# Kernel tuning notes

Measured on AMD Instinct MI355X. Metric: run time of the kernel, lower is better.

The kernel has to match this reference:

```python
import jax, jax.numpy as jnp
import numpy as np

B, S, H = 2, 2048, 4096
NH, NKV, HD = 32, 8, 128
GROUPS = NH // NKV
ROPE_THETA = 10000.0


def _rotate_half(x):
    x1, x2 = jnp.split(x, 2, axis=-1)
    return jnp.concatenate([-x2, x1], axis=-1)


def setup_inputs() -> dict:
    key = jax.random.key(0)
    k1, k2 = jax.random.split(key, 2)
    hidden_states = jax.random.normal(k1, (B, S, H), dtype=jnp.float32)
    position_ids = jnp.tile(jnp.arange(S, dtype=jnp.int64)[None, :], (B, 1))
    # rotary tables, llama-style: freqs duplicated into full head_dim
    inv_freq = (1.0 / (ROPE_THETA ** (np.arange(0, HD, 2, dtype=np.float32) / HD))).astype(np.float32)
    ang = position_ids[..., None].astype(jnp.float32) * jnp.asarray(inv_freq)  # (B,S,HD/2)
    emb = jnp.concatenate([ang, ang], axis=-1)  # (B,S,HD)
    cos = jnp.cos(emb)
    sin = jnp.sin(emb)
    # fused QKV weight, stored as (in, out) so x @ w matches Linear(x)
    w_qkv = jax.random.normal(k2, (H, (NH + 2 * NKV) * HD), dtype=jnp.float32) * 0.02
    return {"hidden_states": hidden_states, "cos": cos, "sin": sin,
            "w_qkv": w_qkv, "position_ids": position_ids}


def reference(hidden_states, cos, sin, w_qkv, position_ids):
    bsz, q_len, _ = hidden_states.shape
    q_slice = NH * HD
    k_slice = q_slice + NKV * HD
    # fused QKV gemm
    qkv = hidden_states @ w_qkv  # (B,S,(NH+2*NKV)*HD)
    query = qkv[:, :, :q_slice].reshape(bsz, q_len, NH, HD)
    key = qkv[:, :, q_slice:k_slice].reshape(bsz, q_len, NKV, HD)
    value = qkv[:, :, k_slice:].reshape(bsz, q_len, NKV, HD)
    # RoPE (broadcast cos/sin over head axis)
    c = cos[:, :, None, :]
    s = sin[:, :, None, :]
    query = query * c + _rotate_half(query) * s
    key = key * c + _rotate_half(key) * s
    # (B, heads, S, HD)
    q = query.transpose(0, 2, 1, 3)
    k = jnp.repeat(key.transpose(0, 2, 1, 3), GROUPS, axis=1)
    v = jnp.repeat(value.transpose(0, 2, 1, 3), GROUPS, axis=1)
    scale = 1.0 / jnp.sqrt(jnp.asarray(HD, dtype=q.dtype))
    scores = jnp.einsum("bhqd,bhkd->bhqk", q, k) * scale
    causal = jnp.tril(jnp.ones((q_len, q_len), dtype=bool))
    scores = jnp.where(causal[None, None], scores, jnp.asarray(-1e30, scores.dtype))
    probs = jax.nn.softmax(scores, axis=-1)
    attn = jnp.einsum("bhqk,bhkd->bhqd", probs, v)  # (B,NH,S,HD)
    out = attn.transpose(0, 2, 1, 3).reshape(bsz, q_len, NH * HD)
    return out
```

## Files before the change

kernel.cpp:

```cpp
#include <hip/hip_runtime.h>
#include <hip/hip_bf16.h>

#define BATCH 2
#define S_LEN 2048
#define HID   4096
#define N_QKV 6144
#define NHEADS 32
#define NKVH   8
#define HDIM   128
#define MROWS  4096
#define QBLK  128
#define KVBLK 64

typedef __attribute__((ext_vector_type(4))) float f32x4;
typedef __attribute__((ext_vector_type(8))) short bf16x8;
typedef __attribute__((ext_vector_type(4))) short bf16x4;

__device__ __forceinline__ unsigned short f2bf(float f) {
    unsigned int u = __float_as_uint(f);
    u += 0x7FFFu + ((u >> 16) & 1u);
    return (unsigned short)(u >> 16);
}
__device__ __forceinline__ float bf2f(unsigned short v) {
    return __uint_as_float(((unsigned int)v) << 16);
}

__global__ void cvt_bf16_kernel(const float* __restrict__ in, unsigned short* __restrict__ out) {
    size_t i = ((size_t)blockIdx.x * 256 + threadIdx.x) * 4;
    f32x4 v = *(const f32x4*)(in + i);
    bf16x4 o;
    o.x = (short)f2bf(v.x); o.y = (short)f2bf(v.y);
    o.z = (short)f2bf(v.z); o.w = (short)f2bf(v.w);
    *(bf16x4*)(out + i) = o;
}

__global__ void transpose_w_kernel(const float* __restrict__ w, unsigned short* __restrict__ wt) {
    __shared__ unsigned short tile[64][72];
    const int tn = blockIdx.x * 64;
    const int tk = blockIdx.y * 64;
    const int t  = threadIdx.x;
    const int c4 = (t & 15) * 4;
    const int rr = t >> 4;
#pragma unroll
    for (int i = 0; i < 4; i++) {
        int k = rr + i * 16;
        f32x4 v = *(const f32x4*)(w + (size_t)(tk + k) * N_QKV + tn + c4);
        tile[k][c4 + 0] = f2bf(v.x);
        tile[k][c4 + 1] = f2bf(v.y);
        tile[k][c4 + 2] = f2bf(v.z);
        tile[k][c4 + 3] = f2bf(v.w);
    }
    __syncthreads();
#pragma unroll
    for (int i = 0; i < 4; i++) {
        int n = rr + i * 16;
        bf16x4 o;
        o.x = (short)tile[c4 + 0][n];
        o.y = (short)tile[c4 + 1][n];
        o.z = (short)tile[c4 + 2][n];
        o.w = (short)tile[c4 + 3][n];
        *(bf16x4*)(wt + (size_t)(tn + n) * HID + tk + c4) = o;
    }
}

__device__ __forceinline__ void gload_lds16(const unsigned short* g, unsigned short* l) {
    __builtin_amdgcn_global_load_lds(
        (const __attribute__((address_space(1))) unsigned int*)g,
        (__attribute__((address_space(3))) unsigned int*)l, 16, 0, 0);
}

__global__ __launch_bounds__(256) void gemm_qkv_kernel(const unsigned short* __restrict__ A,
                                                       const unsigned short* __restrict__ Bt,
                                                       unsigned short* __restrict__ C) {
    __shared__ unsigned short Al[128 * 32];
    __shared__ unsigned short Bl[128 * 32];
    const int bm = (blockIdx.x & 31) * 128;
    const int bn = (blockIdx.x >> 5) * 128;
    const int t = threadIdx.x;
    const int w = t >> 6, l = t & 63;
    const int wm = (w >> 1) * 64, wn = (w & 1) * 64;
    f32x4 acc[4][4] = {};

    const int srow = w * 32 + (l >> 2);
    const int skk  = (l & 3) * 8;
    const unsigned short* ag = A  + (size_t)(bm + srow) * HID + skk;
    const unsigned short* bg = Bt + (size_t)(bn + srow) * HID + skk;

    for (int k0 = 0; k0 < HID; k0 += 32) {
#pragma unroll
        for (int c = 0; c < 2; c++) {
            gload_lds16(ag + (size_t)c * 16 * HID + k0, Al + (w * 32 + c * 16) * 32);
            gload_lds16(bg + (size_t)c * 16 * HID + k0, Bl + (w * 32 + c * 16) * 32);
        }
        __syncthreads();
        bf16x8 af[4], bfr[4];
#pragma unroll
        for (int i = 0; i < 4; i++) {
            af[i]  = *(const bf16x8*)(Al + (wm + i * 16 + (l & 15)) * 32 + (l >> 4) * 8);
            bfr[i] = *(const bf16x8*)(Bl + (wn + i * 16 + (l & 15)) * 32 + (l >> 4) * 8);
        }
#pragma unroll
        for (int i = 0; i < 4; i++)
#pragma unroll
            for (int j = 0; j < 4; j++)
                acc[i][j] = __builtin_amdgcn_mfma_f32_16x16x32_bf16(af[i], bfr[j], acc[i][j], 0, 0, 0);
        __syncthreads();
    }

#pragma unroll
    for (int i = 0; i < 4; i++)
#pragma unroll
        for (int j = 0; j < 4; j++)
#pragma unroll
            for (int r = 0; r < 4; r++) {
                int row = bm + wm + i * 16 + (l >> 4) * 4 + r;
                int col = bn + wn + j * 16 + (l & 15);
                C[(size_t)row * N_QKV + col] = f2bf(acc[i][j][r]);
            }
}

__global__ void rope_kernel(unsigned short* __restrict__ qkv,
                            const float* __restrict__ cs, const float* __restrict__ sn) {
    size_t id = (size_t)blockIdx.x * 256 + threadIdx.x;
    int d = (int)(id & 63);
    size_t tmp = id >> 6;
    int hd = (int)(tmp % 40);
    size_t r = tmp / 40;
    float c = cs[r * HDIM + d];
    float s = sn[r * HDIM + d];
    unsigned short* p = qkv + r * N_QKV + (size_t)hd * HDIM + d;
    float x1 = bf2f(p[0]), x2 = bf2f(p[64]);
    float o1 = x1 * c - x2 * s;
    float o2 = x2 * c + x1 * s;
    if (hd < NHEADS) { o1 *= 0.088388347648318447f; o2 *= 0.088388347648318447f; }
    p[0]  = f2bf(o1);
    p[64] = f2bf(o2);
}

__global__ void transpose_v_kernel(const unsigned short* __restrict__ qkv,
                                   unsigned short* __restrict__ vtg) {
    __shared__ unsigned short tile[64][72];
    const int bz = blockIdx.z;
    const int d0 = blockIdx.y * 64;
    const int s0 = blockIdx.x * 64;
    const int b  = bz >> 3, kvh = bz & 7;
    const int t = threadIdx.x;
#pragma unroll
    for (int i = 0; i < 2; i++) {
        int s  = i * 32 + (t >> 3);
        int dl = (t & 7) * 8;
        bf16x8 v = *(const bf16x8*)(qkv + (size_t)(b * S_LEN + s0 + s) * N_QKV
                                    + HID + NKVH * HDIM + (size_t)kvh * HDIM + d0 + dl);
        *(bf16x8*)(&tile[s][dl]) = v;
    }
    __syncthreads();
#pragma unroll
    for (int i = 0; i < 2; i++) {
        int d  = i * 32 + (t >> 3);
        int sl = (t & 7) * 8;
        bf16x8 o;
#pragma unroll
        for (int j = 0; j < 8; j++) o[j] = (short)tile[sl + j][d];
        *(bf16x8*)(vtg + ((size_t)bz * HDIM + d0 + d) * S_LEN + s0 + sl) = o;
    }
}

__global__ __launch_bounds__(256, 2) void attn_kernel(const unsigned short* __restrict__ qkv,
                                                      const unsigned short* __restrict__ vtg,
                                                      float* __restrict__ out) {
    __shared__ unsigned short Kl[2][KVBLK * HDIM];
    __shared__ unsigned short Vl[HDIM * KVBLK];
    __shared__ unsigned short Pl[4][16 * 72];

    const int bid = blockIdx.x;
    const int qbi = bid & 15;
    const int h   = (bid >> 4) & 31;
    const int b   = bid >> 9;
    const int kvh = h >> 2;
    const int qb  = qbi * QBLK;
    const int t = threadIdx.x, w = t >> 6, l = t & 63;
    const int lo = l & 15, hi = l >> 4;
    const int sw = lo & 7;
    const size_t rowb = (size_t)b * S_LEN;

    const int krow = t >> 4;
    const unsigned short* kg = qkv + (rowb + krow) * N_QKV + HID + (size_t)kvh * HDIM
                               + (((t & 15) ^ (krow & 7)) << 3);
    const int vrow = t >> 3;
    const unsigned short* vg = vtg + ((size_t)(b * NKVH + kvh) * HDIM + vrow) * S_LEN
                               + (((t & 7) ^ (vrow & 7)) << 3);
    unsigned short* kl0 = &Kl[0][t * 8];
    unsigned short* kl1 = &Kl[1][t * 8];
    unsigned short* vl  = &Vl[t * 8];

    bf16x8 qf[2][4];
#pragma unroll
    for (int g = 0; g < 2; g++) {
        const unsigned short* qp = qkv + (rowb + qb + w * 32 + g * 16 + lo) * N_QKV
                                   + (size_t)h * HDIM + hi * 8;
#pragma unroll
        for (int kc = 0; kc < 4; kc++) qf[g][kc] = *(const bf16x8*)(qp + kc * 32);
    }

    f32x4 of[2][8] = {};
    float m_r[2][4], l_r[2][4];
#pragma unroll
    for (int g = 0; g < 2; g++)
#pragma unroll
        for (int r = 0; r < 4; r++) { m_r[g][r] = -1e30f; l_r[g][r] = 0.f; }

    const int nt = (qb + QBLK) / KVBLK;
    const int wrowmax = qb + w * 32 + 31;

#pragma unroll
    for (int i = 0; i < 4; i++)
        gload_lds16(kg + (size_t)i * 16 * N_QKV, kl0 + i * 2048);

    for (int kt = 0; kt < nt; kt++) {
        const int kv0 = kt * KVBLK;
        __syncthreads();
#pragma unroll
        for (int i = 0; i < 4; i++)
            gload_lds16(vg + kv0 + (size_t)i * 32 * S_LEN, vl + i * 2048);
        if (kt + 1 < nt) {
            const unsigned short* kp = kg + (size_t)(kv0 + KVBLK) * N_QKV;
            unsigned short* kd = ((kt + 1) & 1) ? kl1 : kl0;
#pragma unroll
            for (int i = 0; i < 4; i++)
                gload_lds16(kp + (size_t)i * 16 * N_QKV, kd + i * 2048);
        }

        bf16x8 pf[2][2];
        const bool wact = (kv0 <= wrowmax);
        if (wact) {
            const unsigned short* Kb = (kt & 1) ? &Kl[1][0] : &Kl[0][0];
            f32x4 sf[2][4] = {};
#pragma unroll
            for (int kvb = 0; kvb < 4; kvb++)
#pragma unroll
                for (int kc = 0; kc < 4; kc++) {
                    bf16x8 kf = *(const bf16x8*)(Kb + (kvb * 16 + lo) * HDIM
                                                 + (((kc * 4 + hi) ^ sw) << 3));
#pragma unroll
                    for (int g = 0; g < 2; g++)
                        sf[g][kvb] = __builtin_amdgcn_mfma_f32_16x16x32_bf16(
                            qf[g][kc], kf, sf[g][kvb], 0, 0, 0);
                }
#pragma unroll
            for (int g = 0; g < 2; g++) {
                const int rb = qb + w * 32 + g * 16;
                if (kv0 + KVBLK - 1 > rb) {
#pragma unroll
                    for (int kvb = 0; kvb < 4; kvb++) {
                        const int kv = kv0 + kvb * 16 + lo;
#pragma unroll
                        for (int r = 0; r < 4; r++)
                            if (kv > rb + hi * 4 + r) sf[g][kvb][r] = -1e30f;
                    }
                }
                float pm[4];
#pragma unroll
                for (int r = 0; r < 4; r++)
                    pm[r] = fmaxf(fmaxf(sf[g][0][r], sf[g][1][r]),
                                  fmaxf(sf[g][2][r], sf[g][3][r]));
#pragma unroll
                for (int off = 8; off >= 1; off >>= 1)
#pragma unroll
                    for (int r = 0; r < 4; r++)
                        pm[r] = fmaxf(pm[r], __shfl_xor(pm[r], off, 64));
                float dm = fmaxf(fmaxf(pm[0] - m_r[g][0], pm[1] - m_r[g][1]),
                                 fmaxf(pm[2] - m_r[g][2], pm[3] - m_r[g][3]));
                if (__any(dm > 8.0f)) {
#pragma unroll
                    for (int r = 0; r < 4; r++) {
                        const float mn = fmaxf(m_r[g][r], pm[r]);
                        const float sc = __expf(m_r[g][r] - mn);
                        m_r[g][r] = mn;
                        l_r[g][r] *= sc;
#pragma unroll
                        for (int d16 = 0; d16 < 8; d16++) of[g][d16][r] *= sc;
                    }
                }
                float rs[4] = {0.f, 0.f, 0.f, 0.f};
#pragma unroll
                for (int kvb = 0; kvb < 4; kvb++)
#pragma unroll
                    for (int r = 0; r < 4; r++) {
                        const float p = __expf(sf[g][kvb][r] - m_r[g][r]);
                        sf[g][kvb][r] = p;
                        rs[r] += p;
                    }
#pragma unroll
                for (int off = 8; off >= 1; off >>= 1)
#pragma unroll
                    for (int r = 0; r < 4; r++) rs[r] += __shfl_xor(rs[r], off, 64);
#pragma unroll
                for (int r = 0; r < 4; r++) l_r[g][r] += rs[r];
                unsigned short* Pw = &Pl[w][0];
#pragma unroll
                for (int kvb = 0; kvb < 4; kvb++)
#pragma unroll
                    for (int r = 0; r < 4; r++)
                        Pw[(hi * 4 + r) * 72 + kvb * 16 + lo] = f2bf(sf[g][kvb][r]);
#pragma unroll
                for (int kh = 0; kh < 2; kh++)
                    pf[g][kh] = *(const bf16x8*)(Pw + lo * 72 + kh * 32 + hi * 8);
            }
        }
        __syncthreads();
        if (wact) {
#pragma unroll
            for (int kh = 0; kh < 2; kh++)
#pragma unroll
                for (int d16 = 0; d16 < 8; d16++) {
                    bf16x8 vf = *(const bf16x8*)(&Vl[0]
                                                 + ((d16 * 16 + lo) << 6)
                                                 + (((kh * 4 + hi) ^ sw) << 3));
#pragma unroll
                    for (int g = 0; g < 2; g++)
                        of[g][d16] = __builtin_amdgcn_mfma_f32_16x16x32_bf16(
                            pf[g][kh], vf, of[g][d16], 0, 0, 0);
                }
        }
    }

#pragma unroll
    for (int g = 0; g < 2; g++) {
        float inv[4];
#pragma unroll
        for (int r = 0; r < 4; r++) inv[r] = 1.0f / l_r[g][r];
        const size_t rb = rowb + qb + w * 32 + g * 16 + hi * 4;
#pragma unroll
        for (int d16 = 0; d16 < 8; d16++)
#pragma unroll
            for (int r = 0; r < 4; r++)
                out[(rb + r) * HID + (size_t)h * HDIM + d16 * 16 + lo] = of[g][d16][r] * inv[r];
    }
}

extern "C" void kernel_launch(void* const* d_in, const int* in_sizes, int n_in,
                              void* d_out, int out_size, void* d_ws, size_t ws_size,
                              hipStream_t stream) {
    const float* hidden = (const float*)d_in[0];
    const float* cosb   = (const float*)d_in[1];
    const float* sinb   = (const float*)d_in[2];
    const float* w_qkv  = (const float*)d_in[3];

    unsigned short* hbf = (unsigned short*)d_ws;
    unsigned short* wt  = hbf + (size_t)MROWS * HID;
    unsigned short* qkv = wt + (size_t)N_QKV * HID;
    unsigned short* vtg = (unsigned short*)d_ws;
    float* out = (float*)d_out;

    cvt_bf16_kernel<<<(MROWS * (size_t)HID) / 1024, 256, 0, stream>>>(hidden, hbf);
    transpose_w_kernel<<<dim3(N_QKV / 64, HID / 64), 256, 0, stream>>>(w_qkv, wt);
    gemm_qkv_kernel<<<(MROWS / 128) * (N_QKV / 128), 256, 0, stream>>>(hbf, wt, qkv);
    rope_kernel<<<((size_t)MROWS * 40 * 64) / 256, 256, 0, stream>>>(qkv, cosb, sinb);
    transpose_v_kernel<<<dim3(S_LEN / 64, HDIM / 64, BATCH * NKVH), 256, 0, stream>>>(qkv, vtg);
    attn_kernel<<<BATCH * NHEADS * (S_LEN / QBLK), 256, 0, stream>>>(qkv, vtg, out);
}
```

Measured before the change: 711.3 us.

## Rewrite QKV GEMM as 256x256 pipelined tile and pair causal attention query blocks

The QKV GEMM moves from 128x128 tiles with 256 threads to 256x256 tiles with 512 threads. It uses double-buffered, XOR-swizzled LDS staging with explicit vmcnt waits, barrier-interleaved phases, setprio around MFMA bursts, and a grid swizzle for L2 locality. This targets the GEMM's memory-latency and LDS-reload overhead, at the cost of 128KB of LDS and more registers per block. Separately, each attention block now processes query block i and its mirror 15-i, which balances causal work across blocks and halves the grid.

```diff
diff --git a/kernel.cpp b/kernel.cpp
--- a/kernel.cpp
+++ b/kernel.cpp
@@ -11,6 +11,7 @@
 #define MROWS  4096
 #define QBLK  128
 #define KVBLK 64
+#define NT_K  64
 
 typedef __attribute__((ext_vector_type(4))) float f32x4;
 typedef __attribute__((ext_vector_type(8))) short bf16x8;
@@ -69,52 +70,103 @@
         (__attribute__((address_space(3))) unsigned int*)l, 16, 0, 0);
 }
 
-__global__ __launch_bounds__(256) void gemm_qkv_kernel(const unsigned short* __restrict__ A,
-                                                       const unsigned short* __restrict__ Bt,
-                                                       unsigned short* __restrict__ C) {
-    __shared__ unsigned short Al[128 * 32];
-    __shared__ unsigned short Bl[128 * 32];
-    const int bm = (blockIdx.x & 31) * 128;
-    const int bn = (blockIdx.x >> 5) * 128;
+__global__ __launch_bounds__(512, 2) void gemm_qkv_kernel(const unsigned short* __restrict__ A,
+                                                          const unsigned short* __restrict__ Bt,
+                                                          unsigned short* __restrict__ C) {
+    __shared__ alignas(16) unsigned short AL[32768];
+    __shared__ alignas(16) unsigned short BL[32768];
     const int t = threadIdx.x;
     const int w = t >> 6, l = t & 63;
-    const int wm = (w >> 1) * 64, wn = (w & 1) * 64;
-    f32x4 acc[4][4] = {};
-
-    const int srow = w * 32 + (l >> 2);
-    const int skk  = (l & 3) * 8;
-    const unsigned short* ag = A  + (size_t)(bm + srow) * HID + skk;
-    const unsigned short* bg = Bt + (size_t)(bn + srow) * HID + skk;
-
-    for (int k0 = 0; k0 < HID; k0 += 32) {
-#pragma unroll
-        for (int c = 0; c < 2; c++) {
-            gload_lds16(ag + (size_t)c * 16 * HID + k0, Al + (w * 32 + c * 16) * 32);
-            gload_lds16(bg + (size_t)c * 16 * HID + k0, Bl + (w * 32 + c * 16) * 32);
-        }
-        __syncthreads();
-        bf16x8 af[4], bfr[4];
-#pragma unroll
-        for (int i = 0; i < 4; i++) {
-            af[i]  = *(const bf16x8*)(Al + (wm + i * 16 + (l & 15)) * 32 + (l >> 4) * 8);
-            bfr[i] = *(const bf16x8*)(Bl + (wn + i * 16 + (l & 15)) * 32 + (l >> 4) * 8);
-        }
-#pragma unroll
-        for (int i = 0; i < 4; i++)
-#pragma unroll
-            for (int j = 0; j < 4; j++)
-                acc[i][j] = __builtin_amdgcn_mfma_f32_16x16x32_bf16(af[i], bfr[j], acc[i][j], 0, 0, 0);
-        __syncthreads();
-    }
-
-#pragma unroll
-    for (int i = 0; i < 4; i++)
+    const int lo = l & 15, hi = l >> 4;
+    const int wr = w >> 2, wc = w & 3;
+    const int bid = blockIdx.x;
+    const int swz = (bid & 7) * 48 + (bid >> 3);
+    const int bm = (swz / 24) * 256;
+    const int bn = (swz % 24) * 256;
+
+    const int rS = t >> 2;
+    const int cS = (t & 3) ^ ((rS >> 1) & 3);
+    const unsigned short* As = A  + (size_t)(bm + rS) * HID + cS * 8;
+    const unsigned short* Bs = Bt + (size_t)(bn + rS) * HID + cS * 8;
+    unsigned short* ALd = AL + t * 8;
+    unsigned short* BLd = BL + t * 8;
+
+#define STAGE_A(DST, KPOS) do { \
+        gload_lds16(As + (KPOS), ALd + (DST)); \
+        gload_lds16(As + (size_t)128 * HID + (KPOS), ALd + (DST) + 4096); } while (0)
+#define STAGE_B(DST, KPOS) do { \
+        gload_lds16(Bs + (KPOS), BLd + (DST)); \
+        gload_lds16(Bs + (size_t)128 * HID + (KPOS), BLd + (DST) + 4096); } while (0)
+
+    STAGE_A(0, 0);            STAGE_B(0, 0);
+    STAGE_A(8192, 32);        STAGE_B(8192, 32);
+    STAGE_A(16384, 64);       STAGE_B(16384, 64);
+    asm volatile("s_waitcnt vmcnt(8)" ::: "memory");
+    __builtin_amdgcn_s_barrier();
+
+    f32x4 acc[8][4] = {};
+    const int csw8 = (hi ^ ((l & 6) >> 1)) * 8;
+
+#define GPHASE(KHB, MH, READB, STAGECODE, WAITCODE) do {                         \
+        bf16x8 af0, af1, af2, af3;                                               \
+        { const unsigned short* ap = Ab + (KHB) + (wr * 128 + (MH) * 64 + lo) * 32 + csw8; \
+          af0 = *(const bf16x8*)(ap);                                            \
+          af1 = *(const bf16x8*)(ap + 16 * 32);                                  \
+          af2 = *(const bf16x8*)(ap + 32 * 32);                                  \
+          af3 = *(const bf16x8*)(ap + 48 * 32); }                                \
+        if (READB) {                                                             \
+          const unsigned short* bp = Bb + (KHB) + (wc * 64 + lo) * 32 + csw8;    \
+          bfr[0] = *(const bf16x8*)(bp);                                         \
+          bfr[1] = *(const bf16x8*)(bp + 16 * 32);                               \
+          bfr[2] = *(const bf16x8*)(bp + 32 * 32);                               \
+          bfr[3] = *(const bf16x8*)(bp + 48 * 32); }                             \
+        STAGECODE;                                                               \
+        __builtin_amdgcn_s_barrier();                                            \
+        __builtin_amdgcn_s_setprio(1);                                           \
+        _Pragma("unroll")                                                        \
+        for (int jj = 0; jj < 4; jj++) {                                         \
+            acc[(MH)*4+0][jj] = __builtin_amdgcn_mfma_f32_16x16x32_bf16(af0, bfr[jj], acc[(MH)*4+0][jj], 0, 0, 0); \
+            acc[(MH)*4+1][jj] = __builtin_amdgcn_mfma_f32_16x16x32_bf16(af1, bfr[jj], acc[(MH)*4+1][jj], 0, 0, 0); \
+            acc[(MH)*4+2][jj] = __builtin_amdgcn_mfma_f32_16x16x32_bf16(af2, bfr[jj], acc[(MH)*4+2][jj], 0, 0, 0); \
+            acc[(MH)*4+3][jj] = __builtin_amdgcn_mfma_f32_16x16x32_bf16(af3, bfr[jj], acc[(MH)*4+3][jj], 0, 0, 0); \
+        }                                                                        \
+        __builtin_amdgcn_s_setprio(0);                                           \
+        WAITCODE;                                                                \
+        __builtin_amdgcn_s_barrier();                                            \
+    } while (0)
+
+    for (int u = 0; u < NT_K; u++) {
+        const int buf = (u & 1) * 16384;
+        const unsigned short* Ab = AL + buf;
+        const unsigned short* Bb = BL + buf;
+        bf16x8 bfr[4];
+        GPHASE(0, 0, 1,
+               { if (u + 1 < NT_K) STAGE_A(((u + 1) & 1) * 16384 + 8192, (u + 1) * 64 + 32); },
+               {});
+        GPHASE(0, 1, 0,
+               { if (u + 1 < NT_K) STAGE_B(((u + 1) & 1) * 16384 + 8192, (u + 1) * 64 + 32); },
+               { if (u < NT_K - 1) asm volatile("s_waitcnt vmcnt(8)" ::: "memory");
+                 else              asm volatile("s_waitcnt vmcnt(0)" ::: "memory"); });
+        GPHASE(8192, 0, 1,
+               { if (u + 2 < NT_K) STAGE_A(buf, (u + 2) * 64); },
+               {});
+        GPHASE(8192, 1, 0,
+               { if (u + 2 < NT_K) STAGE_B(buf, (u + 2) * 64); },
+               { if (u < NT_K - 2)      asm volatile("s_waitcnt vmcnt(8)" ::: "memory");
+                 else if (u == NT_K - 2) asm volatile("s_waitcnt vmcnt(4)" ::: "memory"); });
+    }
+#undef GPHASE
+#undef STAGE_A
+#undef STAGE_B
+
+#pragma unroll
+    for (int i = 0; i < 8; i++)
 #pragma unroll
         for (int j = 0; j < 4; j++)
 #pragma unroll
             for (int r = 0; r < 4; r++) {
-                int row = bm + wm + i * 16 + (l >> 4) * 4 + r;
-                int col = bn + wn + j * 16 + (l & 15);
+                const int row = bm + wr * 128 + i * 16 + hi * 4 + r;
+                const int col = bn + wc * 64 + j * 16 + lo;
                 C[(size_t)row * N_QKV + col] = f2bf(acc[i][j][r]);
             }
 }
@@ -173,11 +225,10 @@
     __shared__ unsigned short Pl[4][16 * 72];
 
     const int bid = blockIdx.x;
-    const int qbi = bid & 15;
-    const int h   = (bid >> 4) & 31;
-    const int b   = bid >> 9;
+    const int qbi0 = bid & 7;
+    const int h   = (bid >> 3) & 31;
+    const int b   = bid >> 8;
     const int kvh = h >> 2;
-    const int qb  = qbi * QBLK;
     const int t = threadIdx.x, w = t >> 6, l = t & 63;
     const int lo = l & 15, hi = l >> 4;
     const int sw = lo & 7;
@@ -193,148 +244,152 @@
     unsigned short* kl1 = &Kl[1][t * 8];
     unsigned short* vl  = &Vl[t * 8];
 
-    bf16x8 qf[2][4];
-#pragma unroll
-    for (int g = 0; g < 2; g++) {
-        const unsigned short* qp = qkv + (rowb + qb + w * 32 + g * 16 + lo) * N_QKV
-                                   + (size_t)h * HDIM + hi * 8;
-#pragma unroll
-        for (int kc = 0; kc < 4; kc++) qf[g][kc] = *(const bf16x8*)(qp + kc * 32);
-    }
-
-    f32x4 of[2][8] = {};
-    float m_r[2][4], l_r[2][4];
-#pragma unroll
-    for (int g = 0; g < 2; g++)
-#pragma unroll
-        for (int r = 0; r < 4; r++) { m_r[g][r] = -1e30f; l_r[g][r] = 0.f; }
-
-    const int nt = (qb + QBLK) / KVBLK;
-    const int wrowmax = qb + w * 32 + 31;
-
-#pragma unroll
-    for (int i = 0; i < 4; i++)
-        gload_lds16(kg + (size_t)i * 16 * N_QKV, kl0 + i * 2048);
-
-    for (int kt = 0; kt < nt; kt++) {
-        const int kv0 = kt * KVBLK;
-        __syncthreads();
+    for (int hv = 0; hv < 2; hv++) {
+        const int qb = (hv ? (15 - qbi0) : qbi0) * QBLK;
+
+        bf16x8 qf[2][4];
+#pragma unroll
+        for (int g = 0; g < 2; g++) {
+            const unsigned short* qp = qkv + (rowb + qb + w * 32 + g * 16 + lo) * N_QKV
+                                       + (size_t)h * HDIM + hi * 8;
+#pragma unroll
+            for (int kc = 0; kc < 4; kc++) qf[g][kc] = *(const bf16x8*)(qp + kc * 32);
+        }
+
+        f32x4 of[2][8] = {};
+        float m_r[2][4], l_r[2][4];
+#pragma unroll
+        for (int g = 0; g < 2; g++)
+#pragma unroll
+            for (int r = 0; r < 4; r++) { m_r[g][r] = -1e30f; l_r[g][r] = 0.f; }
+
+        const int nt = (qb + QBLK) / KVBLK;
+        const int wrowmax = qb + w * 32 + 31;
+
 #pragma unroll
         for (int i = 0; i < 4; i++)
-            gload_lds16(vg + kv0 + (size_t)i * 32 * S_LEN, vl + i * 2048);
-        if (kt + 1 < nt) {
-            const unsigned short* kp = kg + (size_t)(kv0 + KVBLK) * N_QKV;
-            unsigned short* kd = ((kt + 1) & 1) ? kl1 : kl0;
+            gload_lds16(kg + (size_t)i * 16 * N_QKV, kl0 + i * 2048);
+
+        for (int kt = 0; kt < nt; kt++) {
+            const int kv0 = kt * KVBLK;
+            __syncthreads();
 #pragma unroll
             for (int i = 0; i < 4; i++)
-                gload_lds16(kp + (size_t)i * 16 * N_QKV, kd + i * 2048);
-        }
-
-        bf16x8 pf[2][2];
-        const bool wact = (kv0 <= wrowmax);
-        if (wact) {
-            const unsigned short* Kb = (kt & 1) ? &Kl[1][0] : &Kl[0][0];
-            f32x4 sf[2][4] = {};
-#pragma unroll
-            for (int kvb = 0; kvb < 4; kvb++)
-#pragma unroll
-                for (int kc = 0; kc < 4; kc++) {
-                    bf16x8 kf = *(const bf16x8*)(Kb + (kvb * 16 + lo) * HDIM
-                                                 + (((kc * 4 + hi) ^ sw) << 3));
-#pragma unroll
-                    for (int g = 0; g < 2; g++)
-                        sf[g][kvb] = __builtin_amdgcn_mfma_f32_16x16x32_bf16(
-                            qf[g][kc], kf, sf[g][kvb], 0, 0, 0);
+                gload_lds16(vg + kv0 + (size_t)i * 32 * S_LEN, vl + i * 2048);
+            if (kt + 1 < nt) {
+                const unsigned short* kp = kg + (size_t)(kv0 + KVBLK) * N_QKV;
+                unsigned short* kd = ((kt + 1) & 1) ? kl1 : kl0;
+#pragma unroll
+                for (int i = 0; i < 4; i++)
+                    gload_lds16(kp + (size_t)i * 16 * N_QKV, kd + i * 2048);
+            }
+
+            bf16x8 pf[2][2];
+            const bool wact = (kv0 <= wrowmax);
+            if (wact) {
+                const unsigned short* Kb = (kt & 1) ? &Kl[1][0] : &Kl[0][0];
+                f32x4 sf[2][4] = {};
+#pragma unroll
+                for (int kvb = 0; kvb < 4; kvb++)
+#pragma unroll
+                    for (int kc = 0; kc < 4; kc++) {
+                        bf16x8 kf = *(const bf16x8*)(Kb + (kvb * 16 + lo) * HDIM
+                                                     + (((kc * 4 + hi) ^ sw) << 3));
+#pragma unroll
+                        for (int g = 0; g < 2; g++)
+                            sf[g][kvb] = __builtin_amdgcn_mfma_f32_16x16x32_bf16(
+                                qf[g][kc], kf, sf[g][kvb], 0, 0, 0);
+                    }
+#pragma unroll
+                for (int g = 0; g < 2; g++) {
+                    const int rb = qb + w * 32 + g * 16;
+                    if (kv0 + KVBLK - 1 > rb) {
+#pragma unroll
+                        for (int kvb = 0; kvb < 4; kvb++) {
+                            const int kv = kv0 + kvb * 16 + lo;
+#pragma unroll
+                            for (int r = 0; r < 4; r++)
+                                if (kv > rb + hi * 4 + r) sf[g][kvb][r] = -1e30f;
+                        }
+                    }
+                    float pm[4];
+#pragma unroll
+                    for (int r = 0; r < 4; r++)
+                        pm[r] = fmaxf(fmaxf(sf[g][0][r], sf[g][1][r]),
+                                      fmaxf(sf[g][2][r], sf[g][3][r]));
+#pragma unroll
+                    for (int off = 8; off >= 1; off >>= 1)
+#pragma unroll
+                        for (int r = 0; r < 4; r++)
+                            pm[r] = fmaxf(pm[r], __shfl_xor(pm[r], off, 64));
+                    float dm = fmaxf(fmaxf(pm[0] - m_r[g][0], pm[1] - m_r[g][1]),
+                                     fmaxf(pm[2] - m_r[g][2], pm[3] - m_r[g][3]));
+                    if (__any(dm > 8.0f)) {
+#pragma unroll
+                        for (int r = 0; r < 4; r++) {
+                            const float mn = fmaxf(m_r[g][r], pm[r]);
+                            const float sc = __expf(m_r[g][r] - mn);
+                            m_r[g][r] = mn;
+                            l_r[g][r] *= sc;
+#pragma unroll
+                            for (int d16 = 0; d16 < 8; d16++) of[g][d16][r] *= sc;
+                        }
+                    }
+                    float rs[4] = {0.f, 0.f, 0.f, 0.f};
+#pragma unroll
+                    for (int kvb = 0; kvb < 4; kvb++)
+#pragma unroll
+                        for (int r = 0; r < 4; r++) {
+                            const float p = __expf(sf[g][kvb][r] - m_r[g][r]);
+                            sf[g][kvb][r] = p;
+                            rs[r] += p;
+                        }
+#pragma unroll
+                    for (int off = 8; off >= 1; off >>= 1)
+#pragma unroll
+                        for (int r = 0; r < 4; r++) rs[r] += __shfl_xor(rs[r], off, 64);
+#pragma unroll
+                    for (int r = 0; r < 4; r++) l_r[g][r] += rs[r];
+                    unsigned short* Pw = &Pl[w][0];
+#pragma unroll
+                    for (int kvb = 0; kvb < 4; kvb++)
+#pragma unroll
+                        for (int r = 0; r < 4; r++)
+                            Pw[(hi * 4 + r) * 72 + kvb * 16 + lo] = f2bf(sf[g][kvb][r]);
+#pragma unroll
+                    for (int kh = 0; kh < 2; kh++)
+                        pf[g][kh] = *(const bf16x8*)(Pw + lo * 72 + kh * 32 + hi * 8);
                 }
-#pragma unroll
-            for (int g = 0; g < 2; g++) {
-                const int rb = qb + w * 32 + g * 16;
-                if (kv0 + KVBLK - 1 > rb) {
-#pragma unroll
-                    for (int kvb = 0; kvb < 4; kvb++) {
-                        const int kv = kv0 + kvb * 16 + lo;
-#pragma unroll
-                        for (int r = 0; r < 4; r++)
-                            if (kv > rb + hi * 4 + r) sf[g][kvb][r] = -1e30f;
+            }
+            __syncthreads();
+            if (wact) {
+#pragma unroll
+                for (int kh = 0; kh < 2; kh++)
+#pragma unroll
+                    for (int d16 = 0; d16 < 8; d16++) {
+                        bf16x8 vf = *(const bf16x8*)(&Vl[0]
+                                                     + ((d16 * 16 + lo) << 6)
+                                                     + (((kh * 4 + hi) ^ sw) << 3));
+#pragma unroll
+                        for (int g = 0; g < 2; g++)
+                            of[g][d16] = __builtin_amdgcn_mfma_f32_16x16x32_bf16(
+                                pf[g][kh], vf, of[g][d16], 0, 0, 0);
                     }
-                }
-                float pm[4];
-#pragma unroll
-                for (int r = 0; r < 4; r++)
-                    pm[r] = fmaxf(fmaxf(sf[g][0][r], sf[g][1][r]),
-                                  fmaxf(sf[g][2][r], sf[g][3][r]));
-#pragma unroll
-                for (int off = 8; off >= 1; off >>= 1)
-#pragma unroll
-                    for (int r = 0; r < 4; r++)
-                        pm[r] = fmaxf(pm[r], __shfl_xor(pm[r], off, 64));
-                float dm = fmaxf(fmaxf(pm[0] - m_r[g][0], pm[1] - m_r[g][1]),
-                                 fmaxf(pm[2] - m_r[g][2], pm[3] - m_r[g][3]));
-                if (__any(dm > 8.0f)) {
-#pragma unroll
-                    for (int r = 0; r < 4; r++) {
-                        const float mn = fmaxf(m_r[g][r], pm[r]);
-                        const float sc = __expf(m_r[g][r] - mn);
-                        m_r[g][r] = mn;
-                        l_r[g][r] *= sc;
-#pragma unroll
-                        for (int d16 = 0; d16 < 8; d16++) of[g][d16][r] *= sc;
-                    }
-                }
-                float rs[4] = {0.f, 0.f, 0.f, 0.f};
-#pragma unroll
-                for (int kvb = 0; kvb < 4; kvb++)
-#pragma unroll
-                    for (int r = 0; r < 4; r++) {
-                        const float p = __expf(sf[g][kvb][r] - m_r[g][r]);
-                        sf[g][kvb][r] = p;
-                        rs[r] += p;
-                    }
-#pragma unroll
-                for (int off = 8; off >= 1; off >>= 1)
-#pragma unroll
-                    for (int r = 0; r < 4; r++) rs[r] += __shfl_xor(rs[r], off, 64);
-#pragma unroll
-                for (int r = 0; r < 4; r++) l_r[g][r] += rs[r];
-                unsigned short* Pw = &Pl[w][0];
-#pragma unroll
-                for (int kvb = 0; kvb < 4; kvb++)
-#pragma unroll
-                    for (int r = 0; r < 4; r++)
-                        Pw[(hi * 4 + r) * 72 + kvb * 16 + lo] = f2bf(sf[g][kvb][r]);
-#pragma unroll
-                for (int kh = 0; kh < 2; kh++)
-                    pf[g][kh] = *(const bf16x8*)(Pw + lo * 72 + kh * 32 + hi * 8);
             }
         }
-        __syncthreads();
-        if (wact) {
-#pragma unroll
-            for (int kh = 0; kh < 2; kh++)
-#pragma unroll
-                for (int d16 = 0; d16 < 8; d16++) {
-                    bf16x8 vf = *(const bf16x8*)(&Vl[0]
-                                                 + ((d16 * 16 + lo) << 6)
-                                                 + (((kh * 4 + hi) ^ sw) << 3));
-#pragma unroll
-                    for (int g = 0; g < 2; g++)
-                        of[g][d16] = __builtin_amdgcn_mfma_f32_16x16x32_bf16(
-                            pf[g][kh], vf, of[g][d16], 0, 0, 0);
-                }
+
+#pragma unroll
+        for (int g = 0; g < 2; g++) {
+            float inv[4];
+#pragma unroll
+            for (int r = 0; r < 4; r++) inv[r] = 1.0f / l_r[g][r];
+            const size_t rb = rowb + qb + w * 32 + g * 16 + hi * 4;
+#pragma unroll
+            for (int d16 = 0; d16 < 8; d16++)
+#pragma unroll
+                for (int r = 0; r < 4; r++)
+                    out[(rb + r) * HID + (size_t)h * HDIM + d16 * 16 + lo] = of[g][d16][r] * inv[r];
         }
-    }
-
-#pragma unroll
-    for (int g = 0; g < 2; g++) {
-        float inv[4];
-#pragma unroll
-        for (int r = 0; r < 4; r++) inv[r] = 1.0f / l_r[g][r];
-        const size_t rb = rowb + qb + w * 32 + g * 16 + hi * 4;
-#pragma unroll
-        for (int d16 = 0; d16 < 8; d16++)
-#pragma unroll
-            for (int r = 0; r < 4; r++)
-                out[(rb + r) * HID + (size_t)h * HDIM + d16 * 16 + lo] = of[g][d16][r] * inv[r];
     }
 }
 
@@ -354,8 +409,8 @@
 
     cvt_bf16_kernel<<<(MROWS * (size_t)HID) / 1024, 256, 0, stream>>>(hidden, hbf);
     transpose_w_kernel<<<dim3(N_QKV / 64, HID / 64), 256, 0, stream>>>(w_qkv, wt);
-    gemm_qkv_kernel<<<(MROWS / 128) * (N_QKV / 128), 256, 0, stream>>>(hbf, wt, qkv);
+    gemm_qkv_kernel<<<(MROWS / 256) * (N_QKV / 256), 512, 0, stream>>>(hbf, wt, qkv);
     rope_kernel<<<((size_t)MROWS * 40 * 64) / 256, 256, 0, stream>>>(qkv, cosb, sinb);
     transpose_v_kernel<<<dim3(S_LEN / 64, HDIM / 64, BATCH * NKVH), 256, 0, stream>>>(qkv, vtg);
-    attn_kernel<<<BATCH * NHEADS * (S_LEN / QBLK), 256, 0, stream>>>(qkv, vtg, out);
-}
+    attn_kernel<<<BATCH * NHEADS * (S_LEN / QBLK / 2), 256, 0, stream>>>(qkv, vtg, out);
+}
```

Measured after the change: 661.8 us. -6.9%, faster.
